# Kernel optimization log

Measured on AMD Instinct MI355X. Metric: run time of the kernel, lower is better.

## Reference

```python
import jax, jax.numpy as jnp
import numpy as np


def smooth_l1(x, y):
    d = jnp.abs(x - y)
    return jnp.where(d < 1.0, 0.5 * d * d, d - 0.5)


def setup_inputs() -> dict:
    key = jax.random.key(0)
    k1, k2, k3 = jax.random.split(key, 3)
    B, T, N, D = 4, 28, 1024, 3
    X_v = jax.random.normal(k1, (B, T, N, D), dtype=jnp.float32)
    target_X_v = jax.random.normal(k2, (B, T, N, D), dtype=jnp.float32)
    weights = jax.random.uniform(k3, (B, T), dtype=jnp.float32)
    return {"X_v": X_v, "target_X_v": target_X_v, "weights": weights}


def reference(X_v, target_X_v, weights):
    B = X_v.shape[0]
    # Pairwise squared distances [B,T,N,N] via ||p||^2 + ||t||^2 - 2 p.t
    pn = jnp.sum(X_v * X_v, axis=-1)                 # [B,T,N]
    tn = jnp.sum(target_X_v * target_X_v, axis=-1)   # [B,T,N]
    dist = (pn[..., :, None] + tn[..., None, :]
            - 2.0 * jnp.einsum('btnd,btmd->btnm', X_v, target_X_v))
    minv = jnp.argmin(dist, axis=-1)                 # [B,T,N] int
    # gather nearest target point for each pred point
    tagp = jnp.take_along_axis(target_X_v, minv[..., None], axis=2)  # [B,T,N,3]
    # per-(b,t) mean smooth-L1 over N points x 3 coords
    loss_bt = jnp.mean(smooth_l1(X_v, tagp), axis=(-2, -1))          # [B,T]
    loss = jnp.sum(loss_bt * weights) / B

    prec = jnp.mean(X_v, axis=2)        # [B,T,3]
    tarc = jnp.mean(target_X_v, axis=2) # [B,T,3]
    lossc = jnp.sum(smooth_l1(prec, tarc)) / (B * 3)
    return (loss, lossc)
```

## Files before the change

kernel.cpp:

```cpp
#include <hip/hip_runtime.h>

constexpr int Bc = 4;
constexpr int Tc = 28;
constexpr int Nc = 1024;
constexpr int Dc = 3;
constexpr int BT = Bc * Tc;
constexpr int HALF = 512;
constexpr float OFFS = 512.0f;

__device__ __forceinline__ float sl1(float d) {
    d = fabsf(d);
    return d < 1.0f ? 0.5f * d * d : d - 0.5f;
}

__device__ __forceinline__ float blockSum(float v, int tid, float* scratch) {
    #pragma unroll
    for (int off = 32; off; off >>= 1) v += __shfl_down(v, off, 64);
    if ((tid & 63) == 0) scratch[tid >> 6] = v;
    __syncthreads();
    float r = scratch[0] + scratch[1] + scratch[2] + scratch[3];
    __syncthreads();
    return r;
}

__global__ __launch_bounds__(256) void chamfer_part_kernel(
    const float* __restrict__ X, const float* __restrict__ Tg,
    unsigned long long* __restrict__ keys, float* __restrict__ cent)
{
    __shared__ float sRaw[HALF * 3];
    __shared__ float4 sT4[HALF];
    __shared__ float sred[4];

    const int bt  = blockIdx.x >> 2;
    const int ph  = (blockIdx.x >> 1) & 1;
    const int th  = blockIdx.x & 1;
    const int tid = threadIdx.x;

    const float* tg = Tg + (size_t)bt * (Nc * Dc) + th * (HALF * 3);
    const float4* tg4 = (const float4*)tg;
    float4* sR4 = (float4*)sRaw;
    #pragma unroll
    for (int i = 0; i < (HALF * 3 / 4) / 256 + 1; ++i) {
        int j = tid + i * 256;
        if (j < HALF * 3 / 4) sR4[j] = tg4[j];
    }
    __syncthreads();

    float x0 = sRaw[6 * tid + 0], y0 = sRaw[6 * tid + 1], z0 = sRaw[6 * tid + 2];
    float x1 = sRaw[6 * tid + 3], y1 = sRaw[6 * tid + 4], z1 = sRaw[6 * tid + 5];
    sT4[2 * tid]     = make_float4(x0, y0, z0, fmaf(x0, x0, fmaf(y0, y0, fmaf(z0, z0, OFFS))));
    sT4[2 * tid + 1] = make_float4(x1, y1, z1, fmaf(x1, x1, fmaf(y1, y1, fmaf(z1, z1, OFFS))));
    __syncthreads();

    const float* xb = X + (size_t)bt * (Nc * Dc);
    const int n0 = ph * HALF + tid;
    const int n1 = n0 + 256;
    const float pAx = xb[n0 * 3 + 0], pAy = xb[n0 * 3 + 1], pAz = xb[n0 * 3 + 2];
    const float pBx = xb[n1 * 3 + 0], pBy = xb[n1 * 3 + 1], pBz = xb[n1 * 3 + 2];
    const float cA0 = -2.0f * pAx, cA1 = -2.0f * pAy, cA2 = -2.0f * pAz;
    const float cB0 = -2.0f * pBx, cB1 = -2.0f * pBy, cB2 = -2.0f * pBz;

    float bestA = 3.4e38f, bestB = 3.4e38f;
    int iA = 0, iB = 0;
    #pragma unroll 4
    for (int m = 0; m < HALF; ++m) {
        const float4 t = sT4[m];
        float vA = fmaf(cA0, t.x, fmaf(cA1, t.y, fmaf(cA2, t.z, t.w)));
        float vB = fmaf(cB0, t.x, fmaf(cB1, t.y, fmaf(cB2, t.z, t.w)));
        bool ca = vA < bestA; bestA = ca ? vA : bestA; iA = ca ? m : iA;
        bool cb = vB < bestB; bestB = cb ? vB : bestB; iB = cb ? m : iB;
    }

    const unsigned mbase = th * HALF;
    unsigned long long kA =
        ((unsigned long long)__float_as_uint(bestA) << 32) | (unsigned long long)((unsigned)iA + mbase);
    unsigned long long kB =
        ((unsigned long long)__float_as_uint(bestB) << 32) | (unsigned long long)((unsigned)iB + mbase);
    atomicMin(&keys[(size_t)bt * Nc + n0], kA);
    atomicMin(&keys[(size_t)bt * Nc + n1], kB);

    float psx = blockSum(pAx + pBx, tid, sred);
    float psy = blockSum(pAy + pBy, tid, sred);
    float psz = blockSum(pAz + pBz, tid, sred);
    float tsx = blockSum(x0 + x1, tid, sred);
    float tsy = blockSum(y0 + y1, tid, sred);
    float tsz = blockSum(z0 + z1, tid, sred);
    if (tid == 0) {
        if (th == 0) {
            atomicAdd(&cent[bt * 6 + 0], psx);
            atomicAdd(&cent[bt * 6 + 1], psy);
            atomicAdd(&cent[bt * 6 + 2], psz);
        }
        if (ph == 0) {
            atomicAdd(&cent[bt * 6 + 3], tsx);
            atomicAdd(&cent[bt * 6 + 4], tsy);
            atomicAdd(&cent[bt * 6 + 5], tsz);
        }
    }
}

__global__ __launch_bounds__(256) void finalize_kernel(
    const float* __restrict__ X, const float* __restrict__ Tg,
    const float* __restrict__ W,
    const unsigned long long* __restrict__ keys,
    const float* __restrict__ cent, float* __restrict__ out)
{
    __shared__ float sred[4];
    const int bt  = blockIdx.x >> 2;
    const int tid = threadIdx.x;
    const int n   = ((blockIdx.x & 3) << 8) | tid;

    const float* xb = X  + (size_t)bt * (Nc * Dc);
    const float* tb = Tg + (size_t)bt * (Nc * Dc);

    const unsigned idx = (unsigned)(keys[(size_t)bt * Nc + n] & 0xFFFFFFFFull);
    const float px = xb[n * 3 + 0], py = xb[n * 3 + 1], pz = xb[n * 3 + 2];
    const float tx = tb[idx * 3 + 0], ty = tb[idx * 3 + 1], tz = tb[idx * 3 + 2];
    float s = sl1(px - tx) + sl1(py - ty) + sl1(pz - tz);

    #pragma unroll
    for (int off = 32; off; off >>= 1) s += __shfl_down(s, off, 64);
    if ((tid & 63) == 0) sred[tid >> 6] = s;
    __syncthreads();
    if (tid == 0) {
        float tot = sred[0] + sred[1] + sred[2] + sred[3];
        atomicAdd(out, tot * W[bt] * (1.0f / (Nc * Dc)) * (1.0f / Bc));
    }

    if (blockIdx.x == 0 && tid < BT) {
        const float* c = cent + tid * 6;
        const float inv = 1.0f / Nc;
        float l = sl1((c[0] - c[3]) * inv) + sl1((c[1] - c[4]) * inv) + sl1((c[2] - c[5]) * inv);
        atomicAdd(out + 1, l * (1.0f / (Bc * Dc)));
    }
}

extern "C" void kernel_launch(void* const* d_in, const int* in_sizes, int n_in,
                              void* d_out, int out_size, void* d_ws, size_t ws_size,
                              hipStream_t stream) {
    const float* X  = (const float*)d_in[0];
    const float* Tg = (const float*)d_in[1];
    const float* W  = (const float*)d_in[2];
    float* out = (float*)d_out;

    unsigned long long* keys = (unsigned long long*)d_ws;
    const size_t keys_bytes = (size_t)BT * Nc * sizeof(unsigned long long);
    float* cent = (float*)((char*)d_ws + keys_bytes);

    hipMemsetAsync(out, 0, 2 * sizeof(float), stream);
    hipMemsetAsync(keys, 0xFF, keys_bytes, stream);
    hipMemsetAsync(cent, 0, BT * 6 * sizeof(float), stream);

    chamfer_part_kernel<<<BT * 4, 256, 0, stream>>>(X, Tg, keys, cent);
    finalize_kernel<<<BT * 4, 256, 0, stream>>>(X, Tg, W, keys, cent, out);
}
```

Before: 100.1 us.

## Fuse argmin, gather and loss into one kernel; drop atomics and memsets

Each block now loads all 1024 target points into shared memory and scans the full set, so the argmin no longer needs to be split across blocks and merged with 64-bit atomicMin keys. The smooth-L1 gather and loss are computed in the same kernel from shared memory. Per-block partial sums go to workspace, and a single-block finalize kernel reduces them. This removes three memsets, the keys array traffic and the atomics. The cost is that only 224 blocks run, each scanning twice as many targets, which halves parallelism on a GPU with many CUs.

```diff
diff --git a/kernel.cpp b/kernel.cpp
--- a/kernel.cpp
+++ b/kernel.cpp
@@ -5,65 +5,54 @@
 constexpr int Nc = 1024;
 constexpr int Dc = 3;
 constexpr int BT = Bc * Tc;
-constexpr int HALF = 512;
 constexpr float OFFS = 512.0f;
+
+constexpr int WS_PARTIAL = 0;
+constexpr int WS_PSUM    = 224;
+constexpr int WS_TSUM    = 224 + 224 * 3;
 
 __device__ __forceinline__ float sl1(float d) {
     d = fabsf(d);
     return d < 1.0f ? 0.5f * d * d : d - 0.5f;
 }
 
-__device__ __forceinline__ float blockSum(float v, int tid, float* scratch) {
-    #pragma unroll
-    for (int off = 32; off; off >>= 1) v += __shfl_down(v, off, 64);
-    if ((tid & 63) == 0) scratch[tid >> 6] = v;
-    __syncthreads();
-    float r = scratch[0] + scratch[1] + scratch[2] + scratch[3];
-    __syncthreads();
-    return r;
-}
+__global__ __launch_bounds__(256) void chamfer_kernel(
+    const float* __restrict__ X, const float* __restrict__ Tg,
+    const float* __restrict__ W, float* __restrict__ ws)
+{
+    __shared__ float4 sT4[Nc];
+    __shared__ float sred[4][8];
 
-__global__ __launch_bounds__(256) void chamfer_part_kernel(
-    const float* __restrict__ X, const float* __restrict__ Tg,
-    unsigned long long* __restrict__ keys, float* __restrict__ cent)
-{
-    __shared__ float sRaw[HALF * 3];
-    __shared__ float4 sT4[HALF];
-    __shared__ float sred[4];
-
-    const int bt  = blockIdx.x >> 2;
-    const int ph  = (blockIdx.x >> 1) & 1;
-    const int th  = blockIdx.x & 1;
+    const int bt  = blockIdx.x >> 1;
+    const int ph  = blockIdx.x & 1;
     const int tid = threadIdx.x;
 
-    const float* tg = Tg + (size_t)bt * (Nc * Dc) + th * (HALF * 3);
-    const float4* tg4 = (const float4*)tg;
-    float4* sR4 = (float4*)sRaw;
-    #pragma unroll
-    for (int i = 0; i < (HALF * 3 / 4) / 256 + 1; ++i) {
-        int j = tid + i * 256;
-        if (j < HALF * 3 / 4) sR4[j] = tg4[j];
-    }
-    __syncthreads();
-
-    float x0 = sRaw[6 * tid + 0], y0 = sRaw[6 * tid + 1], z0 = sRaw[6 * tid + 2];
-    float x1 = sRaw[6 * tid + 3], y1 = sRaw[6 * tid + 4], z1 = sRaw[6 * tid + 5];
-    sT4[2 * tid]     = make_float4(x0, y0, z0, fmaf(x0, x0, fmaf(y0, y0, fmaf(z0, z0, OFFS))));
-    sT4[2 * tid + 1] = make_float4(x1, y1, z1, fmaf(x1, x1, fmaf(y1, y1, fmaf(z1, z1, OFFS))));
-    __syncthreads();
-
     const float* xb = X + (size_t)bt * (Nc * Dc);
-    const int n0 = ph * HALF + tid;
+    const int n0 = ph * 512 + tid;
     const int n1 = n0 + 256;
     const float pAx = xb[n0 * 3 + 0], pAy = xb[n0 * 3 + 1], pAz = xb[n0 * 3 + 2];
     const float pBx = xb[n1 * 3 + 0], pBy = xb[n1 * 3 + 1], pBz = xb[n1 * 3 + 2];
+
+    const float4* tg4 = (const float4*)(Tg + (size_t)bt * (Nc * Dc));
+    const float4 r0 = tg4[3 * tid + 0];
+    const float4 r1 = tg4[3 * tid + 1];
+    const float4 r2 = tg4[3 * tid + 2];
+    sT4[4 * tid + 0] = make_float4(r0.x, r0.y, r0.z, fmaf(r0.x, r0.x, fmaf(r0.y, r0.y, fmaf(r0.z, r0.z, OFFS))));
+    sT4[4 * tid + 1] = make_float4(r0.w, r1.x, r1.y, fmaf(r0.w, r0.w, fmaf(r1.x, r1.x, fmaf(r1.y, r1.y, OFFS))));
+    sT4[4 * tid + 2] = make_float4(r1.z, r1.w, r2.x, fmaf(r1.z, r1.z, fmaf(r1.w, r1.w, fmaf(r2.x, r2.x, OFFS))));
+    sT4[4 * tid + 3] = make_float4(r2.y, r2.z, r2.w, fmaf(r2.y, r2.y, fmaf(r2.z, r2.z, fmaf(r2.w, r2.w, OFFS))));
+    const float tsx = r0.x + r0.w + r1.z + r2.y;
+    const float tsy = r0.y + r1.x + r1.w + r2.z;
+    const float tsz = r0.z + r1.y + r2.x + r2.w;
+    __syncthreads();
+
     const float cA0 = -2.0f * pAx, cA1 = -2.0f * pAy, cA2 = -2.0f * pAz;
     const float cB0 = -2.0f * pBx, cB1 = -2.0f * pBy, cB2 = -2.0f * pBz;
 
     float bestA = 3.4e38f, bestB = 3.4e38f;
     int iA = 0, iB = 0;
     #pragma unroll 4
-    for (int m = 0; m < HALF; ++m) {
+    for (int m = 0; m < Nc; ++m) {
         const float4 t = sT4[m];
         float vA = fmaf(cA0, t.x, fmaf(cA1, t.y, fmaf(cA2, t.z, t.w)));
         float vB = fmaf(cB0, t.x, fmaf(cB1, t.y, fmaf(cB2, t.z, t.w)));
@@ -71,67 +60,70 @@
         bool cb = vB < bestB; bestB = cb ? vB : bestB; iB = cb ? m : iB;
     }
 
-    const unsigned mbase = th * HALF;
-    unsigned long long kA =
-        ((unsigned long long)__float_as_uint(bestA) << 32) | (unsigned long long)((unsigned)iA + mbase);
-    unsigned long long kB =
-        ((unsigned long long)__float_as_uint(bestB) << 32) | (unsigned long long)((unsigned)iB + mbase);
-    atomicMin(&keys[(size_t)bt * Nc + n0], kA);
-    atomicMin(&keys[(size_t)bt * Nc + n1], kB);
+    const float4 tA = sT4[iA];
+    const float4 tB = sT4[iB];
+    float s = sl1(pAx - tA.x) + sl1(pAy - tA.y) + sl1(pAz - tA.z)
+            + sl1(pBx - tB.x) + sl1(pBy - tB.y) + sl1(pBz - tB.z);
 
-    float psx = blockSum(pAx + pBx, tid, sred);
-    float psy = blockSum(pAy + pBy, tid, sred);
-    float psz = blockSum(pAz + pBz, tid, sred);
-    float tsx = blockSum(x0 + x1, tid, sred);
-    float tsy = blockSum(y0 + y1, tid, sred);
-    float tsz = blockSum(z0 + z1, tid, sred);
+    float vals[7] = { s, pAx + pBx, pAy + pBy, pAz + pBz, tsx, tsy, tsz };
+    const int lane = tid & 63, wid = tid >> 6;
+    #pragma unroll
+    for (int k = 0; k < 7; ++k) {
+        float v = vals[k];
+        #pragma unroll
+        for (int off = 32; off; off >>= 1) v += __shfl_down(v, off, 64);
+        if (lane == 0) sred[wid][k] = v;
+    }
+    __syncthreads();
     if (tid == 0) {
-        if (th == 0) {
-            atomicAdd(&cent[bt * 6 + 0], psx);
-            atomicAdd(&cent[bt * 6 + 1], psy);
-            atomicAdd(&cent[bt * 6 + 2], psz);
-        }
+        float tot[7];
+        #pragma unroll
+        for (int k = 0; k < 7; ++k)
+            tot[k] = sred[0][k] + sred[1][k] + sred[2][k] + sred[3][k];
+        ws[WS_PARTIAL + blockIdx.x] = tot[0] * W[bt];
+        ws[WS_PSUM + blockIdx.x * 3 + 0] = tot[1];
+        ws[WS_PSUM + blockIdx.x * 3 + 1] = tot[2];
+        ws[WS_PSUM + blockIdx.x * 3 + 2] = tot[3];
         if (ph == 0) {
-            atomicAdd(&cent[bt * 6 + 3], tsx);
-            atomicAdd(&cent[bt * 6 + 4], tsy);
-            atomicAdd(&cent[bt * 6 + 5], tsz);
+            ws[WS_TSUM + bt * 3 + 0] = tot[4];
+            ws[WS_TSUM + bt * 3 + 1] = tot[5];
+            ws[WS_TSUM + bt * 3 + 2] = tot[6];
         }
     }
 }
 
 __global__ __launch_bounds__(256) void finalize_kernel(
-    const float* __restrict__ X, const float* __restrict__ Tg,
-    const float* __restrict__ W,
-    const unsigned long long* __restrict__ keys,
-    const float* __restrict__ cent, float* __restrict__ out)
+    const float* __restrict__ ws, float* __restrict__ out)
 {
-    __shared__ float sred[4];
-    const int bt  = blockIdx.x >> 2;
+    __shared__ float sred[4][2];
     const int tid = threadIdx.x;
-    const int n   = ((blockIdx.x & 3) << 8) | tid;
 
-    const float* xb = X  + (size_t)bt * (Nc * Dc);
-    const float* tb = Tg + (size_t)bt * (Nc * Dc);
+    float lp = (tid < 224) ? ws[WS_PARTIAL + tid] : 0.0f;
 
-    const unsigned idx = (unsigned)(keys[(size_t)bt * Nc + n] & 0xFFFFFFFFull);
-    const float px = xb[n * 3 + 0], py = xb[n * 3 + 1], pz = xb[n * 3 + 2];
-    const float tx = tb[idx * 3 + 0], ty = tb[idx * 3 + 1], tz = tb[idx * 3 + 2];
-    float s = sl1(px - tx) + sl1(py - ty) + sl1(pz - tz);
+    float lc = 0.0f;
+    if (tid < BT) {
+        const float inv = 1.0f / Nc;
+        #pragma unroll
+        for (int c = 0; c < 3; ++c) {
+            float pm = (ws[WS_PSUM + (2 * tid) * 3 + c] + ws[WS_PSUM + (2 * tid + 1) * 3 + c]) * inv;
+            float tm = ws[WS_TSUM + tid * 3 + c] * inv;
+            lc += sl1(pm - tm);
+        }
+    }
 
+    const int lane = tid & 63, wid = tid >> 6;
     #pragma unroll
-    for (int off = 32; off; off >>= 1) s += __shfl_down(s, off, 64);
-    if ((tid & 63) == 0) sred[tid >> 6] = s;
+    for (int off = 32; off; off >>= 1) {
+        lp += __shfl_down(lp, off, 64);
+        lc += __shfl_down(lc, off, 64);
+    }
+    if (lane == 0) { sred[wid][0] = lp; sred[wid][1] = lc; }
     __syncthreads();
     if (tid == 0) {
-        float tot = sred[0] + sred[1] + sred[2] + sred[3];
-        atomicAdd(out, tot * W[bt] * (1.0f / (Nc * Dc)) * (1.0f / Bc));
-    }
-
-    if (blockIdx.x == 0 && tid < BT) {
-        const float* c = cent + tid * 6;
-        const float inv = 1.0f / Nc;
-        float l = sl1((c[0] - c[3]) * inv) + sl1((c[1] - c[4]) * inv) + sl1((c[2] - c[5]) * inv);
-        atomicAdd(out + 1, l * (1.0f / (Bc * Dc)));
+        float tlp = sred[0][0] + sred[1][0] + sred[2][0] + sred[3][0];
+        float tlc = sred[0][1] + sred[1][1] + sred[2][1] + sred[3][1];
+        out[0] = tlp * (1.0f / (Nc * Dc)) * (1.0f / Bc);
+        out[1] = tlc * (1.0f / (Bc * Dc));
     }
 }
 
@@ -142,15 +134,8 @@
     const float* Tg = (const float*)d_in[1];
     const float* W  = (const float*)d_in[2];
     float* out = (float*)d_out;
+    float* ws  = (float*)d_ws;
 
-    unsigned long long* keys = (unsigned long long*)d_ws;
-    const size_t keys_bytes = (size_t)BT * Nc * sizeof(unsigned long long);
-    float* cent = (float*)((char*)d_ws + keys_bytes);
-
-    hipMemsetAsync(out, 0, 2 * sizeof(float), stream);
-    hipMemsetAsync(keys, 0xFF, keys_bytes, stream);
-    hipMemsetAsync(cent, 0, BT * 6 * sizeof(float), stream);
-
-    chamfer_part_kernel<<<BT * 4, 256, 0, stream>>>(X, Tg, keys, cent);
-    finalize_kernel<<<BT * 4, 256, 0, stream>>>(X, Tg, W, keys, cent, out);
+    chamfer_kernel<<<BT * 2, 256, 0, stream>>>(X, Tg, W, ws);
+    finalize_kernel<<<1, 256, 0, stream>>>(ws, out);
 }
```

After: 100.6 us. No clear change (+0.5%).
